# Performance work log

Measured on AMD Instinct MI355X. Metric: run time of the kernel, lower is better.

Reference implementation:

```python
import jax, jax.numpy as jnp
import numpy as np

EMBED_DIM = 1024
NUM_HEADS = 16
HEAD_DIM = EMBED_DIM // NUM_HEADS
SCALING = HEAD_DIM ** -0.5
T, B = 1024, 4


def setup_inputs() -> dict:
    key = jax.random.key(0)
    k1, k2, k3, k4 = jax.random.split(key, 4)
    x_TBC = jax.random.normal(k1, (T, B, EMBED_DIM), dtype=jnp.float32)
    key_padding_mask = jnp.zeros((B, T), dtype=bool)
    edge_bias = jax.random.normal(k2, (B, NUM_HEADS, T, T), dtype=jnp.float32)
    # xavier_uniform-ish init for weights
    lim_qkv = (6.0 / (EMBED_DIM + 3 * EMBED_DIM)) ** 0.5 / (2 ** 0.5)
    w_qkv = jax.random.uniform(k3, (3 * EMBED_DIM, EMBED_DIM), minval=-lim_qkv, maxval=lim_qkv, dtype=jnp.float32)
    b_qkv = jnp.zeros((3 * EMBED_DIM,), dtype=jnp.float32)
    lim_p = (6.0 / (2 * EMBED_DIM)) ** 0.5
    w_proj = jax.random.uniform(k4, (EMBED_DIM, EMBED_DIM), minval=-lim_p, maxval=lim_p, dtype=jnp.float32)
    b_proj = jnp.zeros((EMBED_DIM,), dtype=jnp.float32)
    return {"x_TBC": x_TBC, "key_padding_mask": key_padding_mask, "edge_bias": edge_bias,
            "w_qkv": w_qkv, "b_qkv": b_qkv, "w_proj": w_proj, "b_proj": b_proj}


def reference(x_TBC, key_padding_mask, edge_bias, w_qkv, b_qkv, w_proj, b_proj):
    Tn, Bn, C = x_TBC.shape
    H, Dh = NUM_HEADS, HEAD_DIM
    qkv = x_TBC @ w_qkv.T + b_qkv               # [T,B,3C]
    q, k, v = jnp.split(qkv, 3, axis=-1)
    def split_heads(t):  # [T,B,C] -> [B,H,T,Dh]
        return t.reshape(Tn, Bn, H, Dh).transpose(1, 2, 0, 3)
    q = split_heads(q) * SCALING
    k = split_heads(k)
    v = split_heads(v)
    logits = jnp.einsum('bhtd,bhsd->bhts', q, k) + edge_bias  # [B,H,T,T]
    neg_inf = jnp.finfo(logits.dtype).min
    logits = jnp.where(key_padding_mask[:, None, None, :], neg_inf, logits)
    attn = jax.nn.softmax(logits, axis=-1)
    out = jnp.einsum('bhts,bhsd->bhtd', attn, v)  # [B,H,T,Dh]
    out = out.transpose(2, 0, 1, 3).reshape(Tn, Bn, C)  # [T,B,C]
    out = out @ w_proj.T + b_proj
    return out
```

## Files before the change

### kernel.cpp

```cpp
#include <hip/hip_runtime.h>
#include <stdint.h>
#include <math.h>

#define TT  1024
#define BBN 4
#define CCH 1024
#define HHN 16
#define DHD 64
#define MMR 4096
#define N3  3072

typedef __attribute__((ext_vector_type(4))) float  f32x4;
typedef __attribute__((ext_vector_type(8))) short  s16x8;
typedef __attribute__((ext_vector_type(8))) __bf16 bf16x8;

static __device__ __forceinline__ f32x4 mfma16(s16x8 a, s16x8 b, f32x4 c) {
  return __builtin_amdgcn_mfma_f32_16x16x32_bf16(
      __builtin_bit_cast(bf16x8, a), __builtin_bit_cast(bf16x8, b), c, 0, 0, 0);
}

static __device__ __forceinline__ unsigned short f2bf(float f) {
  union { float f; unsigned int u; } v; v.f = f;
  unsigned int u = v.u;
  return (unsigned short)((u + 0x7FFFu + ((u >> 16) & 1u)) >> 16);
}

typedef const __attribute__((address_space(1))) void GVoid;
typedef __attribute__((address_space(3))) void LVoid;
static __device__ __forceinline__ void gll16(const void* g, void* l) {
  __builtin_amdgcn_global_load_lds((GVoid*)g, (LVoid*)l, 16, 0, 0);
}

#if __has_builtin(__builtin_amdgcn_exp2f)
#define EXP2F(x) __builtin_amdgcn_exp2f(x)
#else
#define EXP2F(x) exp2f(x)
#endif

__global__ void cvt_all(const float* __restrict__ x, const float* __restrict__ wqkv,
                        const float* __restrict__ wproj, unsigned short* __restrict__ out) {
  int i = blockIdx.x * blockDim.x + threadIdx.x;
  const float4* src;
  int off;
  if (i < 1048576)      { src = (const float4*)x;     off = 0; }
  else if (i < 1835008) { src = (const float4*)wqkv;  off = 1048576; }
  else                  { src = (const float4*)wproj; off = 1835008; }
  float4 f = src[i - off];
  ushort4 o;
  o.x = f2bf(f.x); o.y = f2bf(f.y); o.z = f2bf(f.z); o.w = f2bf(f.w);
  ((ushort4*)out)[i] = o;
}

template <int MODE, int BN>
__global__ __launch_bounds__(256, MODE == 0 ? 4 : 3) void gemm_bt(
    const unsigned short* __restrict__ A, const unsigned short* __restrict__ Bw,
    const float* __restrict__ bias, float* __restrict__ Cout,
    unsigned short* __restrict__ qb, unsigned short* __restrict__ kb,
    unsigned short* __restrict__ vtb, int M, int N, int K) {
  constexpr int NI = BN / 32;
  constexpr int AH = 128 * 32;
  constexpr int BH = BN * 32;
  __shared__ __align__(16) unsigned short sMem[3 * AH + 3 * BH];
  unsigned short* sA0 = sMem;
  unsigned short* sB0 = sMem + 3 * AH;
  const int tid = threadIdx.x;
  const int l = tid & 63, w = tid >> 6;
  const int g = l >> 4, c = l & 15;
  const int wr = w >> 1, wc = w & 1;
  const int total = gridDim.x * gridDim.y;
  const int flat = blockIdx.y * gridDim.x + blockIdx.x;
  const int wg = (flat & 7) * (total >> 3) + (flat >> 3);
  const int bxs = wg % gridDim.x, bys = wg / gridDim.x;
  const int bm = bys * 128, bn = bxs * BN;

  const int srow = w * 16 + (l >> 2);
  const int schG = (l & 3) ^ ((l >> 3) & 3);
  const unsigned short* Agp = A + (size_t)(bm + srow) * K + schG * 8;
  const unsigned short* Bgp = Bw + (size_t)(bn + srow) * K + schG * 8;
  const int swzR = (c >> 1) & 3;

  f32x4 acc[4][NI] = {};

#define GSTAGE(s, h) do {                                                        \
    _Pragma("unroll")                                                            \
    for (int i_ = 0; i_ < 2; ++i_)                                               \
      gll16(Agp + (size_t)(i_ * 64) * K + (s) * 32,                              \
            sA0 + (h) * AH + i_ * 2048 + w * 512);                               \
    _Pragma("unroll")                                                            \
    for (int i_ = 0; i_ < BN / 64; ++i_)                                         \
      gll16(Bgp + (size_t)(i_ * 64) * K + (s) * 32,                              \
            sB0 + (h) * BH + i_ * 2048 + w * 512);                               \
  } while (0)

#define GWAIT2 do {                                                              \
    if constexpr (BN == 128) asm volatile("s_waitcnt vmcnt(8)" ::: "memory");    \
    else                     asm volatile("s_waitcnt vmcnt(6)" ::: "memory");    \
  } while (0)
#define GWAIT1 do {                                                              \
    if constexpr (BN == 128) asm volatile("s_waitcnt vmcnt(4)" ::: "memory");    \
    else                     asm volatile("s_waitcnt vmcnt(3)" ::: "memory");    \
  } while (0)

  const int NS = K >> 5;
  GSTAGE(0, 0);
  GSTAGE(1, 1);
  GSTAGE(2, 2);
  GWAIT2;
  __builtin_amdgcn_s_barrier();

  int h = 0;
#pragma unroll 1
  for (int s = 0;; ++s) {
    s16x8 af[4], bfr[NI];
#pragma unroll
    for (int mi = 0; mi < 4; ++mi)
      af[mi] = *(const s16x8*)&sA0[h * AH + (wr * 64 + mi * 16 + c) * 32 + (g ^ swzR) * 8];
#pragma unroll
    for (int ni = 0; ni < NI; ++ni)
      bfr[ni] = *(const s16x8*)&sB0[h * BH + (wc * (BN / 2) + ni * 16 + c) * 32 + (g ^ swzR) * 8];
#pragma unroll
    for (int mi = 0; mi < 4; ++mi)
#pragma unroll
      for (int ni = 0; ni < NI; ++ni)
        acc[mi][ni] = mfma16(af[mi], bfr[ni], acc[mi][ni]);
    if (s == NS - 1) break;
    __builtin_amdgcn_s_barrier();
    if (s + 3 < NS)      { GSTAGE(s + 3, h); GWAIT2; }
    else if (s + 2 < NS) { GWAIT1; }
    else                 { asm volatile("s_waitcnt vmcnt(0)" ::: "memory"); }
    __builtin_amdgcn_s_barrier();
    h = (h == 2) ? 0 : h + 1;
  }

#undef GSTAGE
#undef GWAIT2
#undef GWAIT1

  if (MODE == 1 && (bn >> 10) == 2) {
    unsigned short* sT = sMem;
    const int tl0 = bm >> 2;
#pragma unroll
    for (int pc = 0; pc < 2; ++pc) {
      __syncthreads();
      if (wc == pc) {
#pragma unroll
        for (int mi = 0; mi < 4; ++mi)
#pragma unroll
          for (int ni = 0; ni < NI; ++ni) {
            const int col = bn + pc * 64 + ni * 16 + c;
            const float bsv = bias[col];
#pragma unroll
            for (int j = 0; j < 4; ++j)
              sT[(wr * 64 + mi * 16 + g * 4 + j) * 72 + ni * 16 + c] =
                  f2bf(acc[mi][ni][j] + bsv);
          }
      }
      __syncthreads();
      const int h2 = ((bn + pc * 64) & 1023) >> 6;
      unsigned short* vdst = vtb + ((size_t)(w * 16 + h2) * 64 + l) * 1024 + tl0;
#pragma unroll
      for (int q8 = 0; q8 < 4; ++q8) {
        unsigned short pk[8];
#pragma unroll
        for (int e = 0; e < 8; ++e)
          pk[e] = sT[(((q8 * 8 + e) << 2) | w) * 72 + l];
        *(s16x8*)&vdst[q8 * 8] = *(const s16x8*)pk;
      }
    }
    return;
  }

#pragma unroll
  for (int mi = 0; mi < 4; ++mi)
#pragma unroll
    for (int ni = 0; ni < NI; ++ni) {
      const int col = bn + wc * (BN / 2) + ni * 16 + c;
      const float bsv = bias[col];
      if (MODE == 0) {
#pragma unroll
        for (int j = 0; j < 4; ++j) {
          const int r = bm + wr * 64 + mi * 16 + g * 4 + j;
          Cout[(size_t)r * N + col] = acc[mi][ni][j] + bsv;
        }
      } else {
        const int rem = col & 1023;
        const int hh = rem >> 6, d = rem & 63;
        const bool isq = (col >> 10) == 0;
        const float qscale = 0.18033688f;
#pragma unroll
        for (int j = 0; j < 4; ++j) {
          const int r = bm + wr * 64 + mi * 16 + g * 4 + j;
          const int t = r >> 2, bb = r & 3;
          const int bh = bb * 16 + hh;
          float av = acc[mi][ni][j] + bsv;
          if (isq) qb[((size_t)bh * 1024 + t) * 64 + d] = f2bf(av * qscale);
          else     kb[((size_t)bh * 1024 + t) * 64 + d] = f2bf(av);
        }
      }
    }
}

__global__ __launch_bounds__(256, 3) void attn_kernel(
    const unsigned short* __restrict__ qb, const unsigned short* __restrict__ kb,
    const unsigned short* __restrict__ vtb, const float* __restrict__ eb,
    const unsigned char* __restrict__ mask, unsigned short* __restrict__ ob) {
  __shared__ __align__(16) unsigned short sQ[64 * 64];
  __shared__ __align__(16) unsigned short sK[2][64 * 64];
  __shared__ __align__(16) unsigned short sV[2][64 * 64];
  __shared__ __align__(16) unsigned short sP[4][16 * 72];
  __shared__ __align__(4) unsigned char sM[1024];
  const int tid = threadIdx.x;
  const int l = tid & 63, w = tid >> 6;
  const int g = l >> 4, c = l & 15;
  const int flat = blockIdx.y * 16 + blockIdx.x;
  const int wg = (flat & 7) * 128 + (flat >> 3);
  const int q0 = (wg & 15) * 64;
  const int bh = wg >> 4;
  const int b = bh >> 4;
  const int srow = tid >> 3, sch = tid & 7;

  const unsigned short* qg = qb + (size_t)bh * 65536;
  const unsigned short* kg = kb + (size_t)bh * 65536;
  const unsigned short* vg = vtb + (size_t)bh * 65536;
  const float* ebg = eb + (size_t)bh * 1048576 + (size_t)(q0 + w * 16 + g * 4) * 1024;

  const float BS = 1.44269504f;
  float bvA[4][4], bvB[4][4];
  float ps[4] = {0.f, 0.f, 0.f, 0.f};
  f32x4 po[4] = {};

#define STAGE(tv, P) do {                                                        \
    _Pragma("unroll")                                                            \
    for (int i_ = 0; i_ < 2; ++i_) {                                             \
      int row_ = i_ * 32 + srow;                                                 \
      gll16(kg + (size_t)((tv) * 64 + row_) * 64 + (sch ^ (row_ & 7)) * 8,       \
            &sK[P][i_ * 2048 + w * 512]);                                        \
      gll16(vg + (size_t)row_ * 1024 + (tv) * 64 + (sch ^ (row_ & 7)) * 8,       \
            &sV[P][i_ * 2048 + w * 512]);                                        \
    } } while (0)

#define BIAS(tv, BV) do {                                                        \
    _Pragma("unroll")                                                            \
    for (int ni_ = 0; ni_ < 4; ++ni_)                                            \
      _Pragma("unroll")                                                          \
      for (int j_ = 0; j_ < 4; ++j_)                                             \
        BV[ni_][j_] = ebg[(size_t)j_ * 1024 + (tv) * 64 + ni_ * 16 + c];         \
    } while (0)

#define TILE(P, BV, s0v) do {                                                    \
    float mkc_[4];                                                               \
    _Pragma("unroll")                                                            \
    for (int ni_ = 0; ni_ < 4; ++ni_)                                            \
      mkc_[ni_] = sM[(s0v) + ni_ * 16 + c] ? -1e30f : -8.0f;                     \
    s16x8 kf_[4][2];                                                             \
    _Pragma("unroll")                                                            \
    for (int ni_ = 0; ni_ < 4; ++ni_)                                            \
      _Pragma("unroll")                                                          \
      for (int k2_ = 0; k2_ < 2; ++k2_) {                                        \
        int row_ = ni_ * 16 + c;                                                 \
        kf_[ni_][k2_] = *(const s16x8*)&sK[P][row_ * 64 +                        \
                         (((k2_ * 4 + g) ^ (row_ & 7)) * 8)];                    \
      }                                                                          \
    f32x4 sc_[4] = {};                                                           \
    _Pragma("unroll")                                                            \
    for (int k2_ = 0; k2_ < 2; ++k2_)                                            \
      _Pragma("unroll")                                                          \
      for (int ni_ = 0; ni_ < 4; ++ni_)                                          \
        sc_[ni_] = mfma16(qf[k2_], kf_[ni_][k2_], sc_[ni_]);                     \
    _Pragma("unroll")                                                            \
    for (int ni_ = 0; ni_ < 4; ++ni_)                                            \
      _Pragma("unroll")                                                          \
      for (int j_ = 0; j_ < 4; ++j_) {                                           \
        float x_ = fmaf(BV[ni_][j_], BS, sc_[ni_][j_]) + mkc_[ni_];              \
        float p_ = EXP2F(x_);                                                    \
        sP[w][(g * 4 + j_) * 72 + ni_ * 16 + c] = f2bf(p_);                      \
        ps[j_] += p_;                                                            \
      }                                                                          \
    s16x8 vf_[4][2];                                                             \
    _Pragma("unroll")                                                            \
    for (int nd_ = 0; nd_ < 4; ++nd_)                                            \
      _Pragma("unroll")                                                          \
      for (int k2_ = 0; k2_ < 2; ++k2_) {                                        \
        int row_ = nd_ * 16 + c;                                                 \
        vf_[nd_][k2_] = *(const s16x8*)&sV[P][row_ * 64 +                        \
                         (((k2_ * 4 + g) ^ (row_ & 7)) * 8)];                    \
      }                                                                          \
    asm volatile("s_waitcnt lgkmcnt(0)" ::: "memory");                           \
    __builtin_amdgcn_sched_barrier(0);                                           \
    s16x8 pf_[2];                                                                \
    _Pragma("unroll")                                                            \
    for (int k2_ = 0; k2_ < 2; ++k2_)                                            \
      pf_[k2_] = *(const s16x8*)&sP[w][c * 72 + k2_ * 32 + g * 8];               \
    _Pragma("unroll")                                                            \
    for (int k2_ = 0; k2_ < 2; ++k2_)                                            \
      _Pragma("unroll")                                                          \
      for (int nd_ = 0; nd_ < 4; ++nd_)                                          \
        po[nd_] = mfma16(pf_[k2_], vf_[nd_][k2_], po[nd_]);                      \
  } while (0)

#pragma unroll
  for (int i = 0; i < 2; ++i) {
    int row = i * 32 + srow;
    gll16(qg + (size_t)(q0 + row) * 64 + (sch ^ (row & 7)) * 8, &sQ[i * 2048 + w * 512]);
  }
  STAGE(0, 0);
  STAGE(1, 1);
  BIAS(0, bvA);
  BIAS(1, bvB);
  ((unsigned int*)sM)[tid] = ((const unsigned int*)(mask + b * TT))[tid & 255];
  __syncthreads();

  s16x8 qf[2];
#pragma unroll
  for (int kk2 = 0; kk2 < 2; ++kk2) {
    int row = w * 16 + c;
    qf[kk2] = *(const s16x8*)&sQ[row * 64 + (((kk2 * 4 + g) ^ (row & 7)) * 8)];
  }

#pragma unroll 1
  for (int t2 = 0;; t2 += 2) {
    TILE(0, bvA, t2 * 64);
    __builtin_amdgcn_s_barrier();
    if (t2 + 2 < 16) { STAGE(t2 + 2, 0); BIAS(t2 + 2, bvA); }
    if (t2 == 14) { asm volatile("s_waitcnt vmcnt(16)" ::: "memory"); }
    else          { asm volatile("s_waitcnt vmcnt(36)" ::: "memory"); }
    __builtin_amdgcn_s_barrier();
    TILE(1, bvB, t2 * 64 + 64);
    if (t2 == 14) break;
    __builtin_amdgcn_s_barrier();
    STAGE(t2 + 3, 1); BIAS(t2 + 3, bvB);
    asm volatile("s_waitcnt vmcnt(36)" ::: "memory");
    __builtin_amdgcn_s_barrier();
  }

#undef STAGE
#undef BIAS
#undef TILE

#pragma unroll
  for (int j = 0; j < 4; ++j) {
#pragma unroll
    for (int off = 1; off <= 8; off <<= 1)
      ps[j] += __shfl_xor(ps[j], off, 64);
    ps[j] = 1.0f / ps[j];
  }
  const int h = bh & 15;
#pragma unroll
  for (int nd = 0; nd < 4; ++nd)
#pragma unroll
    for (int j = 0; j < 4; ++j) {
      float val = po[nd][j] * ps[j];
      int t = q0 + w * 16 + g * 4 + j;
      ob[((size_t)t * 4 + b) * 1024 + h * 64 + nd * 16 + c] = f2bf(val);
    }
}

extern "C" void kernel_launch(void* const* d_in, const int* in_sizes, int n_in,
                              void* d_out, int out_size, void* d_ws, size_t ws_size,
                              hipStream_t stream) {
  const float* x      = (const float*)d_in[0];
  const unsigned char* mask = (const unsigned char*)d_in[1];
  const float* ebias  = (const float*)d_in[2];
  const float* wqkv   = (const float*)d_in[3];
  const float* bqkv   = (const float*)d_in[4];
  const float* wproj  = (const float*)d_in[5];
  const float* bproj  = (const float*)d_in[6];
  float* out = (float*)d_out;

  char* ws = (char*)d_ws;
  unsigned short* xb    = (unsigned short*)(ws);
  unsigned short* wqkvb = (unsigned short*)(ws + 8388608);
  unsigned short* wpb   = (unsigned short*)(ws + 14680064);
  unsigned short* qbuf  = (unsigned short*)(ws + 16777216);
  unsigned short* kbuf  = (unsigned short*)(ws + 25165824);
  unsigned short* vtbuf = (unsigned short*)(ws + 33554432);
  unsigned short* obuf  = (unsigned short*)(ws + 41943040);

  cvt_all<<<8192, 256, 0, stream>>>(x, wqkv, wproj, xb);

  gemm_bt<1, 128><<<dim3(24, 32), 256, 0, stream>>>(
      xb, wqkvb, bqkv, nullptr, qbuf, kbuf, vtbuf, MMR, N3, 1024);

  attn_kernel<<<dim3(16, 64), 256, 0, stream>>>(
      qbuf, kbuf, vtbuf, ebias, mask, obuf);

  gemm_bt<0, 64><<<dim3(16, 32), 256, 0, stream>>>(
      obuf, wpb, bproj, out, nullptr, nullptr, nullptr, MMR, 1024, 1024);
}
```

Measured before the change: 147.3 us.

## Use dedicated 256x256-tile 512-thread kernel for QKV projection GEMM

Replaces the templated 128x128 QKV GEMM with a dedicated kernel that uses 256x256 output tiles, 8 waves per block and a 3-stage LDS pipeline. The larger tile raises arithmetic intensity and cuts redundant global loads. The grid shrinks from 768 to 192 blocks, which may hurt load balance across the CUs. The V-transpose epilogue is adapted to the larger tile, and the generic GEMM keeps only the projection path.

Measured after the change: 157.5 us. 1.07x slower.

```diff
diff --git a/kernel.cpp b/kernel.cpp
--- a/kernel.cpp
+++ b/kernel.cpp
@@ -51,12 +51,142 @@
   ((ushort4*)out)[i] = o;
 }
 
+__global__ __launch_bounds__(512, 2) void gemm_qkv(
+    const unsigned short* __restrict__ A, const unsigned short* __restrict__ Bw,
+    const float* __restrict__ bias,
+    unsigned short* __restrict__ qb, unsigned short* __restrict__ kb,
+    unsigned short* __restrict__ vtb) {
+  constexpr int K = 1024;
+  constexpr int AH = 256 * 32;
+  constexpr int BH = 256 * 32;
+  __shared__ __align__(16) unsigned short sMem[3 * AH + 3 * BH];
+  unsigned short* sA0 = sMem;
+  unsigned short* sB0 = sMem + 3 * AH;
+  const int tid = threadIdx.x;
+  const int l = tid & 63, w = tid >> 6;
+  const int g = l >> 4, c = l & 15;
+  const int wr = w >> 2, wc = w & 3;
+  const int total = gridDim.x * gridDim.y;
+  const int flat = blockIdx.y * gridDim.x + blockIdx.x;
+  const int wg = (flat & 7) * (total >> 3) + (flat >> 3);
+  const int bxs = wg % gridDim.x, bys = wg / gridDim.x;
+  const int bm = bys * 256, bn = bxs * 256;
+
+  const int srow = tid >> 2;
+  const int schG = (tid & 3) ^ ((tid >> 3) & 3);
+  const unsigned short* Agp = A + (size_t)(bm + srow) * K + schG * 8;
+  const unsigned short* Bgp = Bw + (size_t)(bn + srow) * K + schG * 8;
+  const int swzR = (c >> 1) & 3;
+
+  f32x4 acc[8][4] = {};
+
+#define QSTAGE(s, h) do {                                                        \
+    _Pragma("unroll")                                                            \
+    for (int i_ = 0; i_ < 2; ++i_)                                               \
+      gll16(Agp + (size_t)(i_ * 128) * K + (s) * 32,                             \
+            sA0 + (h) * AH + i_ * 4096 + w * 512);                               \
+    _Pragma("unroll")                                                            \
+    for (int i_ = 0; i_ < 2; ++i_)                                               \
+      gll16(Bgp + (size_t)(i_ * 128) * K + (s) * 32,                             \
+            sB0 + (h) * BH + i_ * 4096 + w * 512);                               \
+  } while (0)
+
+  const int NS = K >> 5;
+  QSTAGE(0, 0);
+  QSTAGE(1, 1);
+  QSTAGE(2, 2);
+  asm volatile("s_waitcnt vmcnt(8)" ::: "memory");
+  __builtin_amdgcn_s_barrier();
+
+  int h = 0;
+#pragma unroll 1
+  for (int s = 0;; ++s) {
+    s16x8 af[8], bfr[4];
+#pragma unroll
+    for (int mi = 0; mi < 8; ++mi)
+      af[mi] = *(const s16x8*)&sA0[h * AH + (wr * 128 + mi * 16 + c) * 32 + (g ^ swzR) * 8];
+#pragma unroll
+    for (int ni = 0; ni < 4; ++ni)
+      bfr[ni] = *(const s16x8*)&sB0[h * BH + (wc * 64 + ni * 16 + c) * 32 + (g ^ swzR) * 8];
+#pragma unroll
+    for (int mi = 0; mi < 8; ++mi)
+#pragma unroll
+      for (int ni = 0; ni < 4; ++ni)
+        acc[mi][ni] = mfma16(af[mi], bfr[ni], acc[mi][ni]);
+    if (s == NS - 1) break;
+    __builtin_amdgcn_s_barrier();
+    if (s + 3 < NS)      { QSTAGE(s + 3, h);
+                           asm volatile("s_waitcnt vmcnt(8)" ::: "memory"); }
+    else if (s + 2 < NS) { asm volatile("s_waitcnt vmcnt(4)" ::: "memory"); }
+    else                 { asm volatile("s_waitcnt vmcnt(0)" ::: "memory"); }
+    __builtin_amdgcn_s_barrier();
+    h = (h == 2) ? 0 : h + 1;
+  }
+
+#undef QSTAGE
+
+  const int part = bn >> 10;
+  if (part != 2) {
+    const bool isq = (part == 0);
+    const float qscale = 0.18033688f;
+#pragma unroll
+    for (int mi = 0; mi < 8; ++mi)
+#pragma unroll
+      for (int ni = 0; ni < 4; ++ni) {
+        const int col = bn + wc * 64 + ni * 16 + c;
+        const float bsv = bias[col];
+        const int rem = col & 1023;
+        const int hh = rem >> 6, d = rem & 63;
+#pragma unroll
+        for (int j = 0; j < 4; ++j) {
+          const int r = bm + wr * 128 + mi * 16 + g * 4 + j;
+          const int t = r >> 2, bb = r & 3;
+          const int bh = bb * 16 + hh;
+          float av = acc[mi][ni][j] + bsv;
+          if (isq) qb[((size_t)bh * 1024 + t) * 64 + d] = f2bf(av * qscale);
+          else     kb[((size_t)bh * 1024 + t) * 64 + d] = f2bf(av);
+        }
+      }
+    return;
+  }
+
+  unsigned short* sT = sMem;
+  const int tl0 = bm >> 2;
+  const int bb = w & 3, th = w >> 2;
+#pragma unroll 1
+  for (int pc = 0; pc < 4; ++pc) {
+    __syncthreads();
+    if (wc == pc) {
+#pragma unroll
+      for (int mi = 0; mi < 8; ++mi)
+#pragma unroll
+        for (int ni = 0; ni < 4; ++ni) {
+          const int col = bn + pc * 64 + ni * 16 + c;
+          const float bsv = bias[col];
+#pragma unroll
+          for (int j = 0; j < 4; ++j)
+            sT[(wr * 128 + mi * 16 + g * 4 + j) * 72 + ni * 16 + c] =
+                f2bf(acc[mi][ni][j] + bsv);
+        }
+    }
+    __syncthreads();
+    const int h2 = ((bn + pc * 64) & 1023) >> 6;
+    unsigned short* vdst = vtb + ((size_t)(bb * 16 + h2) * 64 + l) * 1024 + tl0 + th * 32;
+#pragma unroll
+    for (int q8 = 0; q8 < 4; ++q8) {
+      unsigned short pk[8];
+#pragma unroll
+      for (int e = 0; e < 8; ++e)
+        pk[e] = sT[(((th * 32 + q8 * 8 + e) << 2) | bb) * 72 + l];
+      *(s16x8*)&vdst[q8 * 8] = *(const s16x8*)pk;
+    }
+  }
+}
+
 template <int MODE, int BN>
-__global__ __launch_bounds__(256, MODE == 0 ? 4 : 3) void gemm_bt(
+__global__ __launch_bounds__(256, 4) void gemm_bt(
     const unsigned short* __restrict__ A, const unsigned short* __restrict__ Bw,
-    const float* __restrict__ bias, float* __restrict__ Cout,
-    unsigned short* __restrict__ qb, unsigned short* __restrict__ kb,
-    unsigned short* __restrict__ vtb, int M, int N, int K) {
+    const float* __restrict__ bias, float* __restrict__ Cout, int M, int N, int K) {
   constexpr int NI = BN / 32;
   constexpr int AH = 128 * 32;
   constexpr int BH = BN * 32;
@@ -92,20 +222,11 @@
             sB0 + (h) * BH + i_ * 2048 + w * 512);                               \
   } while (0)
 
-#define GWAIT2 do {                                                              \
-    if constexpr (BN == 128) asm volatile("s_waitcnt vmcnt(8)" ::: "memory");    \
-    else                     asm volatile("s_waitcnt vmcnt(6)" ::: "memory");    \
-  } while (0)
-#define GWAIT1 do {                                                              \
-    if constexpr (BN == 128) asm volatile("s_waitcnt vmcnt(4)" ::: "memory");    \
-    else                     asm volatile("s_waitcnt vmcnt(3)" ::: "memory");    \
-  } while (0)
-
   const int NS = K >> 5;
   GSTAGE(0, 0);
   GSTAGE(1, 1);
   GSTAGE(2, 2);
-  GWAIT2;
+  asm volatile("s_waitcnt vmcnt(6)" ::: "memory");
   __builtin_amdgcn_s_barrier();
 
   int h = 0;
@@ -125,50 +246,15 @@
         acc[mi][ni] = mfma16(af[mi], bfr[ni], acc[mi][ni]);
     if (s == NS - 1) break;
     __builtin_amdgcn_s_barrier();
-    if (s + 3 < NS)      { GSTAGE(s + 3, h); GWAIT2; }
-    else if (s + 2 < NS) { GWAIT1; }
+    if (s + 3 < NS)      { GSTAGE(s + 3, h);
+                           asm volatile("s_waitcnt vmcnt(6)" ::: "memory"); }
+    else if (s + 2 < NS) { asm volatile("s_waitcnt vmcnt(3)" ::: "memory"); }
     else                 { asm volatile("s_waitcnt vmcnt(0)" ::: "memory"); }
     __builtin_amdgcn_s_barrier();
     h = (h == 2) ? 0 : h + 1;
   }
 
 #undef GSTAGE
-#undef GWAIT2
-#undef GWAIT1
-
-  if (MODE == 1 && (bn >> 10) == 2) {
-    unsigned short* sT = sMem;
-    const int tl0 = bm >> 2;
-#pragma unroll
-    for (int pc = 0; pc < 2; ++pc) {
-      __syncthreads();
-      if (wc == pc) {
-#pragma unroll
-        for (int mi = 0; mi < 4; ++mi)
-#pragma unroll
-          for (int ni = 0; ni < NI; ++ni) {
-            const int col = bn + pc * 64 + ni * 16 + c;
-            const float bsv = bias[col];
-#pragma unroll
-            for (int j = 0; j < 4; ++j)
-              sT[(wr * 64 + mi * 16 + g * 4 + j) * 72 + ni * 16 + c] =
-                  f2bf(acc[mi][ni][j] + bsv);
-          }
-      }
-      __syncthreads();
-      const int h2 = ((bn + pc * 64) & 1023) >> 6;
-      unsigned short* vdst = vtb + ((size_t)(w * 16 + h2) * 64 + l) * 1024 + tl0;
-#pragma unroll
-      for (int q8 = 0; q8 < 4; ++q8) {
-        unsigned short pk[8];
-#pragma unroll
-        for (int e = 0; e < 8; ++e)
-          pk[e] = sT[(((q8 * 8 + e) << 2) | w) * 72 + l];
-        *(s16x8*)&vdst[q8 * 8] = *(const s16x8*)pk;
-      }
-    }
-    return;
-  }
 
 #pragma unroll
   for (int mi = 0; mi < 4; ++mi)
@@ -176,26 +262,10 @@
     for (int ni = 0; ni < NI; ++ni) {
       const int col = bn + wc * (BN / 2) + ni * 16 + c;
       const float bsv = bias[col];
-      if (MODE == 0) {
-#pragma unroll
-        for (int j = 0; j < 4; ++j) {
-          const int r = bm + wr * 64 + mi * 16 + g * 4 + j;
-          Cout[(size_t)r * N + col] = acc[mi][ni][j] + bsv;
-        }
-      } else {
-        const int rem = col & 1023;
-        const int hh = rem >> 6, d = rem & 63;
-        const bool isq = (col >> 10) == 0;
-        const float qscale = 0.18033688f;
-#pragma unroll
-        for (int j = 0; j < 4; ++j) {
-          const int r = bm + wr * 64 + mi * 16 + g * 4 + j;
-          const int t = r >> 2, bb = r & 3;
-          const int bh = bb * 16 + hh;
-          float av = acc[mi][ni][j] + bsv;
-          if (isq) qb[((size_t)bh * 1024 + t) * 64 + d] = f2bf(av * qscale);
-          else     kb[((size_t)bh * 1024 + t) * 64 + d] = f2bf(av);
-        }
+#pragma unroll
+      for (int j = 0; j < 4; ++j) {
+        const int r = bm + wr * 64 + mi * 16 + g * 4 + j;
+        Cout[(size_t)r * N + col] = acc[mi][ni][j] + bsv;
       }
     }
 }
@@ -378,12 +448,12 @@
 
   cvt_all<<<8192, 256, 0, stream>>>(x, wqkv, wproj, xb);
 
-  gemm_bt<1, 128><<<dim3(24, 32), 256, 0, stream>>>(
-      xb, wqkvb, bqkv, nullptr, qbuf, kbuf, vtbuf, MMR, N3, 1024);
+  gemm_qkv<<<dim3(12, 16), 512, 0, stream>>>(
+      xb, wqkvb, bqkv, qbuf, kbuf, vtbuf);
 
   attn_kernel<<<dim3(16, 64), 256, 0, stream>>>(
       qbuf, kbuf, vtbuf, ebias, mask, obuf);
 
   gemm_bt<0, 64><<<dim3(16, 32), 256, 0, stream>>>(
-      obuf, wpb, bproj, out, nullptr, nullptr, nullptr, MMR, 1024, 1024);
-}
+      obuf, wpb, bproj, out, MMR, 1024, 1024);
+}
```
